# Kernel optimization log

Measured on AMD Instinct MI355X. Metric: run time of the kernel, lower is better.

## Reference

```python
import jax, jax.numpy as jnp
import numpy as np

NUM_HEADS = 16
GROUP_SIZE = 4
RMS_EPS = 1e-6


def _rope_cos_sin(S, head_dim):
    # matches compute_freqs_cis: freqs = 1/10000**(arange(0,hd,2)/hd), angles = outer(t, freqs)
    inv_freq = 1.0 / (10000.0 ** (jnp.arange(0, head_dim, 2, dtype=jnp.float32) / head_dim))
    t = jnp.arange(S, dtype=jnp.float32)
    angles = t[:, None] * inv_freq[None, :]          # [S, hd/2]
    return jnp.cos(angles), jnp.sin(angles)


def _apply_rope(x, cos, sin):
    # x: [B, S, h, hd]; complex multiply on (even, odd) pairs
    B, S, h, hd = x.shape
    xr = x.reshape(B, S, h, hd // 2, 2)
    x0, x1 = xr[..., 0], xr[..., 1]
    c = cos[None, :, None, :]
    s = sin[None, :, None, :]
    o0 = x0 * c - x1 * s
    o1 = x0 * s + x1 * c
    return jnp.stack([o0, o1], axis=-1).reshape(B, S, h, hd)


def setup_inputs() -> dict:
    key = jax.random.key(0)
    k1, k2, k3 = jax.random.split(key, 3)
    B, S, H = 4, 2048, 2048
    g = GROUP_SIZE
    x = jax.random.normal(k1, (B, S, H), dtype=jnp.float32)
    w_attn = jax.random.normal(k2, (H, H + 2 * H // g), dtype=jnp.float32) * 0.02
    w_proj = jax.random.normal(k3, (H, H), dtype=jnp.float32) * 0.02
    norm_w = jnp.ones((H,), dtype=jnp.float32)
    return {"x": x, "w_attn": w_attn, "w_proj": w_proj, "norm_w": norm_w}


def reference(x, w_attn, w_proj, norm_w):
    B, S, H = x.shape
    nh = NUM_HEADS
    g = GROUP_SIZE
    nkv = nh // g
    hd = H // nh
    ghd = H // g

    qkv = jnp.einsum('bsh,hf->bsf', x, w_attn)
    q = qkv[..., :H].reshape(B, S, nh, hd)
    k = qkv[..., H:H + ghd].reshape(B, S, nkv, hd)
    v = qkv[..., H + ghd:].reshape(B, S, nkv, hd)

    cos, sin = _rope_cos_sin(S, hd)
    q = _apply_rope(q, cos, sin)
    k = _apply_rope(k, cos, sin)

    q = q.transpose(0, 2, 1, 3)                      # [B, nh, S, hd]
    k = jnp.repeat(k.transpose(0, 2, 1, 3), g, axis=1)   # [B, nh, S, hd]
    v = jnp.repeat(v.transpose(0, 2, 1, 3), g, axis=1)

    scale = 1.0 / jnp.sqrt(jnp.float32(hd))
    scores = jnp.einsum('bhqd,bhkd->bhqk', q, k) * scale
    causal = jnp.tril(jnp.ones((S, S), dtype=bool))
    scores = jnp.where(causal[None, None], scores, jnp.finfo(scores.dtype).min)
    attn = jax.nn.softmax(scores, axis=-1)
    y = jnp.einsum('bhqk,bhkd->bhqd', attn, v)       # [B, nh, S, hd]
    y = y.transpose(0, 2, 1, 3).reshape(B, S, H)

    y = jnp.einsum('bsh,ho->bso', y, w_proj)
    # RMSNorm
    rms = jnp.sqrt(jnp.mean(jnp.square(y), axis=-1, keepdims=True) + RMS_EPS)
    return (y / rms) * norm_w
```

## Files before the change

kernel.cpp:

```cpp
#include <hip/hip_runtime.h>

#define DEVI __device__ __forceinline__

using u16 = unsigned short;
using u32 = unsigned int;

typedef __attribute__((ext_vector_type(8))) short short8v;
typedef __attribute__((ext_vector_type(4))) float f32x4;
typedef __attribute__((ext_vector_type(16))) float f32x16;
typedef __attribute__((ext_vector_type(2))) u32 u32x2;
typedef __attribute__((ext_vector_type(4))) u32 u32x4;

DEVI u16 f2b(float f) {
  u32 u = __builtin_bit_cast(u32, f);
  u += 0x7fffu + ((u >> 16) & 1u);
  return (u16)(u >> 16);
}
DEVI float b2f(u16 b) { return __builtin_bit_cast(float, (u32)b << 16); }

DEVI void gload16(const void* g, void* l) {
  __builtin_amdgcn_global_load_lds(
      (const __attribute__((address_space(1))) void*)g,
      (__attribute__((address_space(3))) void*)l, 16, 0, 0);
}

__global__ __launch_bounds__(256) void cvt_x_k(const float* __restrict__ in,
                                               u16* __restrict__ out) {
  size_t i = ((size_t)blockIdx.x * 256 + threadIdx.x) * 8;
  f32x4 a = *(const f32x4*)(in + i);
  f32x4 c = *(const f32x4*)(in + i + 4);
  short8v o;
  o[0] = (short)f2b(a[0]); o[1] = (short)f2b(a[1]);
  o[2] = (short)f2b(a[2]); o[3] = (short)f2b(a[3]);
  o[4] = (short)f2b(c[0]); o[5] = (short)f2b(c[1]);
  o[6] = (short)f2b(c[2]); o[7] = (short)f2b(c[3]);
  *(short8v*)(out + i) = o;
}

__global__ __launch_bounds__(256) void transpose_cvt_k(
    const float* __restrict__ in, u16* __restrict__ out, int R, int Ccols) {
  __shared__ u16 tile[64][65];
  const int r0 = blockIdx.y * 64, c0 = blockIdx.x * 64;
  const int tx = threadIdx.x & 63, ty = threadIdx.x >> 6;
#pragma unroll
  for (int jj = 0; jj < 16; ++jj) {
    int r = ty + jj * 4;
    tile[r][tx] = f2b(in[(size_t)(r0 + r) * Ccols + c0 + tx]);
  }
  __syncthreads();
#pragma unroll
  for (int jj = 0; jj < 16; ++jj) {
    int c = ty + jj * 4;
    out[(size_t)(c0 + c) * R + r0 + tx] = tile[tx][c];
  }
}

__global__ __launch_bounds__(256) void rope_table_k(float* __restrict__ cosT,
                                                    float* __restrict__ sinT) {
  int idx = blockIdx.x * 256 + threadIdx.x;
  int s = idx >> 6, i = idx & 63;
  float inv_freq = expf(-(float)i * (1.0f / 64.0f) * 9.210340371976184f);
  float ang = (float)s * inv_freq;
  cosT[idx] = cosf(ang);
  sinT[idx] = sinf(ang);
}

__global__ __launch_bounds__(256) void rope_scatter_k(
    const u16* __restrict__ qkv, const float* __restrict__ cosT,
    const float* __restrict__ sinT, u16* __restrict__ q_r,
    u16* __restrict__ k_r) {
  const float QS = 0.08838834764831845f * 1.4426950408889634f;
  const int row = blockIdx.x;
  const int b = row >> 11, s = row & 2047;
  const u16* in = qkv + (size_t)row * 3072;
  const float* cp = cosT + s * 64;
  const float* sp = sinT + s * 64;
  for (int p = threadIdx.x; p < 1280; p += 256) {
    int f0 = p * 2;
    u32 pair = *(const u32*)(in + f0);
    float x0 = b2f((u16)(pair & 0xffffu));
    float x1 = b2f((u16)(pair >> 16));
    int d, head;
    u16* dst;
    bool isq = (f0 < 2048);
    if (isq) {
      head = f0 >> 7; d = f0 & 127;
      dst = q_r + (((size_t)(b * 16 + head)) * 2048 + s) * 128 + d;
    } else {
      int idx = f0 - 2048;
      head = idx >> 7; d = idx & 127;
      dst = k_r + (((size_t)(b * 4 + head)) * 2048 + s) * 128 + d;
    }
    int i = d >> 1;
    float c = cp[i], sn = sp[i];
    float o0 = x0 * c - x1 * sn;
    float o1 = x0 * sn + x1 * c;
    if (isq) { o0 *= QS; o1 *= QS; }
    *(u32*)dst = (u32)f2b(o0) | ((u32)f2b(o1) << 16);
  }
}

__global__ __launch_bounds__(256) void v_trans_k(const u16* __restrict__ qkv,
                                                 u16* __restrict__ vT) {
  __shared__ u16 tile[64][65];
  const int s0 = blockIdx.x * 64, d0 = blockIdx.y * 64;
  const int bk = blockIdx.z;
  const int b = bk >> 2, kh = bk & 3;
  const int tx = threadIdx.x & 63, ty = threadIdx.x >> 6;
  const u16* src = qkv + ((size_t)b * 2048) * 3072 + 2560 + kh * 128;
#pragma unroll
  for (int jj = 0; jj < 16; ++jj) {
    int s = ty + jj * 4;
    tile[s][tx] = src[(size_t)(s0 + s) * 3072 + d0 + tx];
  }
  __syncthreads();
  u16* dst = vT + (((size_t)bk * 128 + d0) * 2048) + s0;
#pragma unroll
  for (int jj = 0; jj < 16; ++jj) {
    int dd = ty + jj * 4;
    dst[(size_t)dd * 2048 + tx] = tile[tx][dd];
  }
}

DEVI short8v ldf(const char* half, int r, int slot) {
  return *(const short8v*)(half + r * 64 + (((slot) ^ (r & 3)) << 4));
}

DEVI void stg(const u16* __restrict__ G, int row0, int Kd, int T, int kh,
              char* dst, int t, int w) {
#pragma unroll
  for (int i = 0; i < 2; ++i) {
    int off = i * 8192 + t * 16;
    int r = off >> 6;
    int gs = ((off >> 4) & 3) ^ (r & 3);
    gload16((const char*)G +
                (((size_t)(row0 + r) * Kd) + T * 64 + kh * 32 + gs * 8) * 2,
            dst + i * 8192 + w * 1024);
  }
}

#define VM4 asm volatile("s_waitcnt vmcnt(4)" ::: "memory")
#define PH(P2, KS, CH, STAGE_STMT, TAILWAIT)                                   \
  {                                                                            \
    if ((CH) == 0) {                                                           \
      _Pragma("unroll") for (int mt = 0; mt < 8; ++mt) af[mt] =                \
          ldf(Ab + (P2) * 32768 + (KS) * 16384, wm * 128 + mt * 16 + lo, hi);  \
    }                                                                          \
    bf0 = ldf(Bb + (P2) * 32768 + (KS) * 16384, wn * 64 + (CH) * 32 + lo, hi);\
    bf1 = ldf(Bb + (P2) * 32768 + (KS) * 16384,                                \
              wn * 64 + (CH) * 32 + 16 + lo, hi);                              \
    STAGE_STMT;                                                                \
    __builtin_amdgcn_sched_barrier(0);                                         \
    __builtin_amdgcn_s_barrier();                                              \
    asm volatile("s_waitcnt lgkmcnt(0)" ::: "memory");                         \
    __builtin_amdgcn_sched_barrier(0);                                         \
    __builtin_amdgcn_s_setprio(1);                                             \
    _Pragma("unroll") for (int mt = 0; mt < 8; ++mt) {                         \
      acc[mt][(CH) * 2] = __builtin_amdgcn_mfma_f32_16x16x32_bf16(             \
          af[mt], bf0, acc[mt][(CH) * 2], 0, 0, 0);                            \
      acc[mt][(CH) * 2 + 1] = __builtin_amdgcn_mfma_f32_16x16x32_bf16(         \
          af[mt], bf1, acc[mt][(CH) * 2 + 1], 0, 0, 0);                        \
    }                                                                          \
    __builtin_amdgcn_s_setprio(0);                                             \
    TAILWAIT;                                                                  \
    __builtin_amdgcn_sched_barrier(0);                                         \
    __builtin_amdgcn_s_barrier();                                              \
    __builtin_amdgcn_sched_barrier(0);                                         \
  }

__global__ __launch_bounds__(512, 2) void gemm256_k(const u16* __restrict__ A,
                                                    const u16* __restrict__ BT,
                                                    u16* __restrict__ C, int N,
                                                    int Kd) {
  __shared__ __align__(16) char lds[131072];
  char* Ab = lds;
  char* Bb = lds + 65536;

  const int t = threadIdx.x;
  const int lane = t & 63, lo = lane & 15, hi = lane >> 4;
  const int w = t >> 6, wm = w >> 2, wn = w & 3;

  const int ntx = gridDim.x;
  const int nwg = ntx * gridDim.y;
  const int orig = blockIdx.y * ntx + blockIdx.x;
  const int cpx = nwg >> 3;
  const int swz = (orig & 7) * cpx + (orig >> 3);
  const int m0 = (swz / ntx) * 256, n0 = (swz % ntx) * 256;

  f32x4 acc[8][4];
#pragma unroll
  for (int a = 0; a < 8; ++a)
#pragma unroll
    for (int c = 0; c < 4; ++c) acc[a][c] = (f32x4){0.f, 0.f, 0.f, 0.f};

  short8v af[8], bf0, bf1;

  const int NK = Kd >> 6;
  const int NK2 = NK >> 1;

  stg(A, m0, Kd, 0, 0, Ab + 0, t, w);
  stg(BT, n0, Kd, 0, 0, Bb + 0, t, w);
  stg(A, m0, Kd, 0, 1, Ab + 16384, t, w);
  stg(BT, n0, Kd, 0, 1, Bb + 16384, t, w);
  stg(A, m0, Kd, 1, 0, Ab + 32768, t, w);
  stg(BT, n0, Kd, 1, 0, Bb + 32768, t, w);
  VM4;
  __builtin_amdgcn_sched_barrier(0);
  __builtin_amdgcn_s_barrier();
  __builtin_amdgcn_sched_barrier(0);

  for (int kt2 = 0; kt2 < NK2; ++kt2) {
    int T1v = 2 * kt2 + 1;
    int T2v = 2 * kt2 + 2; if (T2v > NK - 1) T2v = NK - 1;
    int T3v = 2 * kt2 + 3; if (T3v > NK - 1) T3v = NK - 1;
    PH(0, 0, 0, stg(A, m0, Kd, T1v, 1, Ab + 49152, t, w), (void)0);
    PH(0, 0, 1, stg(BT, n0, Kd, T1v, 1, Bb + 49152, t, w), (void)0);
    PH(0, 1, 0, stg(A, m0, Kd, T2v, 0, Ab + 0, t, w), (void)0);
    PH(0, 1, 1, stg(BT, n0, Kd, T2v, 0, Bb + 0, t, w), VM4);
    PH(1, 0, 0, stg(A, m0, Kd, T2v, 1, Ab + 16384, t, w), (void)0);
    PH(1, 0, 1, stg(BT, n0, Kd, T2v, 1, Bb + 16384, t, w), (void)0);
    PH(1, 1, 0, stg(A, m0, Kd, T3v, 0, Ab + 32768, t, w), (void)0);
    PH(1, 1, 1, stg(BT, n0, Kd, T3v, 0, Bb + 32768, t, w), VM4);
  }
  asm volatile("s_waitcnt vmcnt(0)" ::: "memory");

#pragma unroll
  for (int mt = 0; mt < 8; ++mt)
#pragma unroll
    for (int nt = 0; nt < 4; ++nt)
#pragma unroll
      for (int r = 0; r < 4; ++r) {
        int row = m0 + wm * 128 + mt * 16 + hi * 4 + r;
        int col = n0 + wn * 64 + nt * 16 + lo;
        C[(size_t)row * N + col] = f2b(acc[mt][nt][r]);
      }
}

__global__ __launch_bounds__(256, 2) void attn_k(const u16* __restrict__ Q,
                                                 const u16* __restrict__ K,
                                                 const u16* __restrict__ VT,
                                                 u16* __restrict__ Y) {
  __shared__ __align__(16) u16 lK[2][64 * 128];
  __shared__ __align__(16) u16 lV[2][128 * 64];

  const int t = threadIdx.x;
  const int lane = t & 63;
  const int l31 = lane & 31, hb = lane >> 5;
  const int w = t >> 6;

  const int id = blockIdx.x;
  const int xcd = id & 7, pos = id >> 3;
  const int bh = xcd + ((pos >> 4) << 3);
  const int qt = 15 - (pos & 15);
  const int b = bh >> 4, h = bh & 15, kh = h >> 2;

  const size_t qbase = (size_t)(b * 16 + h) * 2048 * 128;
  const size_t kbase = (size_t)(b * 4 + kh) * 2048 * 128;
  const size_t vbase = (size_t)(b * 4 + kh) * 128 * 2048;

  const int q0 = qt * 128;
  const int qrow = q0 + w * 32 + l31;

  short8v qf[8];
#pragma unroll
  for (int j16 = 0; j16 < 8; ++j16)
    qf[j16] = *(const short8v*)(Q + qbase + (size_t)qrow * 128 + j16 * 16 + hb * 8);

  float m_run = -3.0e38f, l_run = 0.f;
  f32x16 oacc[4];
#pragma unroll
  for (int db = 0; db < 4; ++db)
#pragma unroll
    for (int rg = 0; rg < 16; ++rg) oacc[db][rg] = 0.f;

  const int ntile = 2 * qt + 2;

  auto stageK = [&](int buf, int j) {
    const int kv0 = j * 64;
#pragma unroll
    for (int i = 0; i < 4; ++i) {
      int off = i * 4096 + t * 16;
      int r = off >> 8;
      int sl = (off >> 4) & 15;
      int gs = sl ^ (r & 7);
      gload16((const char*)K + (kbase + (size_t)(kv0 + r) * 128 + gs * 8) * 2,
              (char*)lK[buf] + i * 4096 + w * 1024);
    }
  };
  auto stageV = [&](int buf, int j) {
    const int kv0 = j * 64;
#pragma unroll
    for (int i = 0; i < 4; ++i) {
      int off = i * 4096 + t * 16;
      int r = off >> 7;
      int sl = (off >> 4) & 7;
      int gs = sl ^ (r & 7);
      gload16((const char*)VT + (vbase + (size_t)r * 2048 + kv0 + gs * 8) * 2,
              (char*)lV[buf] + i * 4096 + w * 1024);
    }
  };

  auto pv = [&](const char* lVc, const short8v* pa) {
    __builtin_amdgcn_s_setprio(1);
#pragma unroll
    for (int sc = 0; sc < 4; ++sc) {
      const int c = sc * 2 + hb;
#pragma unroll
      for (int db = 0; db < 4; ++db) {
        int vr = db * 32 + l31;
        short8v vf = *(const short8v*)(lVc + vr * 128 + ((c ^ (vr & 7)) << 4));
        oacc[db] = __builtin_amdgcn_mfma_f32_32x32x16_bf16(vf, pa[sc],
                                                           oacc[db], 0, 0, 0);
      }
    }
    __builtin_amdgcn_s_setprio(0);
  };

  stageK(0, 0);
  asm volatile("s_waitcnt vmcnt(0)" ::: "memory");
  __builtin_amdgcn_sched_barrier(0);
  __builtin_amdgcn_s_barrier();
  __builtin_amdgcn_sched_barrier(0);

  short8v pa_prev[4];

  for (int jj = 0; jj < ntile; ++jj) {
    const int cur = jj & 1;
    if (jj + 1 < ntile) stageK(cur ^ 1, jj + 1);
    stageV(cur, jj);

    const char* lKc = (const char*)lK[cur];
    const int kv0 = jj * 64;

    f32x16 sacc[2];
#pragma unroll
    for (int kb = 0; kb < 2; ++kb)
#pragma unroll
      for (int rg = 0; rg < 16; ++rg) sacc[kb][rg] = 0.f;

    __builtin_amdgcn_s_setprio(1);
#pragma unroll
    for (int j16 = 0; j16 < 8; ++j16) {
      const int c = j16 * 2 + hb;
#pragma unroll
      for (int kb = 0; kb < 2; ++kb) {
        int kr = kb * 32 + l31;
        short8v kf = *(const short8v*)(lKc + kr * 256 + ((c ^ (kr & 7)) << 4));
        sacc[kb] = __builtin_amdgcn_mfma_f32_32x32x16_bf16(kf, qf[j16],
                                                           sacc[kb], 0, 0, 0);
      }
    }
    __builtin_amdgcn_s_setprio(0);

    if (jj >= ntile - 2) {
      const int mb = kv0 + 4 * hb - qrow;
#pragma unroll
      for (int kb = 0; kb < 2; ++kb)
#pragma unroll
        for (int rg = 0; rg < 16; ++rg)
          if (mb + kb * 32 + (rg & 3) + 8 * (rg >> 2) > 0)
            sacc[kb][rg] = -1.0e38f;
    }

    float mt0[16];
#pragma unroll
    for (int rg = 0; rg < 16; ++rg) mt0[rg] = fmaxf(sacc[0][rg], sacc[1][rg]);
#pragma unroll
    for (int rg = 0; rg < 8; ++rg) mt0[rg] = fmaxf(mt0[rg], mt0[rg + 8]);
#pragma unroll
    for (int rg = 0; rg < 4; ++rg) mt0[rg] = fmaxf(mt0[rg], mt0[rg + 4]);
    float mx = fmaxf(fmaxf(mt0[0], mt0[1]), fmaxf(mt0[2], mt0[3]));
    mx = fmaxf(mx, __shfl_xor(mx, 32, 64));

    if (jj > 0) pv((const char*)lV[cur ^ 1], pa_prev);

    if (__any(mx > m_run + 8.f)) {
      float mn = fmaxf(m_run, mx);
      float corr = exp2f(m_run - mn);
      m_run = mn;
      l_run *= corr;
#pragma unroll
      for (int db = 0; db < 4; ++db)
#pragma unroll
        for (int rg = 0; rg < 16; ++rg) oacc[db][rg] *= corr;
    }

    float sm0[16];
#pragma unroll
    for (int kb = 0; kb < 2; ++kb)
#pragma unroll
      for (int rg = 0; rg < 16; ++rg)
        sacc[kb][rg] = exp2f(sacc[kb][rg] - m_run);
#pragma unroll
    for (int rg = 0; rg < 16; ++rg) sm0[rg] = sacc[0][rg] + sacc[1][rg];
#pragma unroll
    for (int rg = 0; rg < 8; ++rg) sm0[rg] += sm0[rg + 8];
#pragma unroll
    for (int rg = 0; rg < 4; ++rg) sm0[rg] += sm0[rg + 4];
    float sm = (sm0[0] + sm0[1]) + (sm0[2] + sm0[3]);
    sm += __shfl_xor(sm, 32, 64);
    l_run += sm;

#pragma unroll
    for (int kb = 0; kb < 2; ++kb) {
      u32 pw00, pw01, pw10, pw11, pw20, pw21, pw30, pw31;
      asm("v_cvt_pk_bf16_f32 %0, %1, %2" : "=v"(pw00) : "v"(sacc[kb][0]), "v"(sacc[kb][1]));
      asm("v_cvt_pk_bf16_f32 %0, %1, %2" : "=v"(pw01) : "v"(sacc[kb][2]), "v"(sacc[kb][3]));
      asm("v_cvt_pk_bf16_f32 %0, %1, %2" : "=v"(pw10) : "v"(sacc[kb][4]), "v"(sacc[kb][5]));
      asm("v_cvt_pk_bf16_f32 %0, %1, %2" : "=v"(pw11) : "v"(sacc[kb][6]), "v"(sacc[kb][7]));
      asm("v_cvt_pk_bf16_f32 %0, %1, %2" : "=v"(pw20) : "v"(sacc[kb][8]), "v"(sacc[kb][9]));
      asm("v_cvt_pk_bf16_f32 %0, %1, %2" : "=v"(pw21) : "v"(sacc[kb][10]), "v"(sacc[kb][11]));
      asm("v_cvt_pk_bf16_f32 %0, %1, %2" : "=v"(pw30) : "v"(sacc[kb][12]), "v"(sacc[kb][13]));
      asm("v_cvt_pk_bf16_f32 %0, %1, %2" : "=v"(pw31) : "v"(sacc[kb][14]), "v"(sacc[kb][15]));
      u32x2 a0 = __builtin_amdgcn_permlane32_swap(pw00, pw10, false, false);
      u32x2 a1 = __builtin_amdgcn_permlane32_swap(pw01, pw11, false, false);
      u32x4 wv0; wv0[0] = a0[0]; wv0[1] = a1[0]; wv0[2] = a0[1]; wv0[3] = a1[1];
      pa_prev[kb * 2 + 0] = __builtin_bit_cast(short8v, wv0);
      u32x2 b0 = __builtin_amdgcn_permlane32_swap(pw20, pw30, false, false);
      u32x2 b1 = __builtin_amdgcn_permlane32_swap(pw21, pw31, false, false);
      u32x4 wv1; wv1[0] = b0[0]; wv1[1] = b1[0]; wv1[2] = b0[1]; wv1[3] = b1[1];
      pa_prev[kb * 2 + 1] = __builtin_bit_cast(short8v, wv1);
    }

    asm volatile("s_waitcnt vmcnt(0)" ::: "memory");
    __builtin_amdgcn_sched_barrier(0);
    __builtin_amdgcn_s_barrier();
    __builtin_amdgcn_sched_barrier(0);
  }

  pv((const char*)lV[(ntile - 1) & 1], pa_prev);

  const float inv = 1.0f / l_run;
  u16* yp = Y + ((size_t)b * 2048 + qrow) * 2048 + h * 128;
#pragma unroll
  for (int db = 0; db < 4; ++db)
#pragma unroll
    for (int j = 0; j < 4; ++j) {
      float a0 = oacc[db][4 * j] * inv, a1 = oacc[db][4 * j + 1] * inv;
      float a2 = oacc[db][4 * j + 2] * inv, a3 = oacc[db][4 * j + 3] * inv;
      u32 w0, w1;
      asm("v_cvt_pk_bf16_f32 %0, %1, %2" : "=v"(w0) : "v"(a0), "v"(a1));
      asm("v_cvt_pk_bf16_f32 %0, %1, %2" : "=v"(w1) : "v"(a2), "v"(a3));
      *(u32x2*)(yp + db * 32 + 8 * j + 4 * hb) = (u32x2){w0, w1};
    }
}

__global__ __launch_bounds__(256) void rmsnorm_k(const u16* __restrict__ Yb,
                                                 const float* __restrict__ nw,
                                                 float* __restrict__ out) {
  const int row = blockIdx.x;
  const int t = threadIdx.x;
  const u16* yr = Yb + (size_t)row * 2048 + t * 8;
  short8v v = *(const short8v*)yr;
  float x[8];
  float ss = 0.f;
#pragma unroll
  for (int j = 0; j < 8; ++j) {
    x[j] = b2f((u16)v[j]);
    ss += x[j] * x[j];
  }
#pragma unroll
  for (int dm = 1; dm < 64; dm <<= 1) ss += __shfl_xor(ss, dm, 64);
  __shared__ float red[4];
  if ((t & 63) == 0) red[t >> 6] = ss;
  __syncthreads();
  float tot = red[0] + red[1] + red[2] + red[3];
  float inv = rsqrtf(tot * (1.0f / 2048.0f) + 1e-6f);
  float* op = out + (size_t)row * 2048 + t * 8;
  const float* wp = nw + t * 8;
  f32x4 o0, o1;
#pragma unroll
  for (int j = 0; j < 4; ++j) o0[j] = x[j] * inv * wp[j];
#pragma unroll
  for (int j = 0; j < 4; ++j) o1[j] = x[4 + j] * inv * wp[4 + j];
  *(f32x4*)op = o0;
  *(f32x4*)(op + 4) = o1;
}

extern "C" void kernel_launch(void* const* d_in, const int* in_sizes, int n_in,
                              void* d_out, int out_size, void* d_ws,
                              size_t ws_size, hipStream_t stream) {
  (void)in_sizes; (void)n_in; (void)out_size; (void)ws_size;
  const float* x = (const float*)d_in[0];
  const float* w_attn = (const float*)d_in[1];
  const float* w_proj = (const float*)d_in[2];
  const float* norm_w = (const float*)d_in[3];
  float* out = (float*)d_out;
  char* ws = (char*)d_ws;

  size_t off = 0;
  auto alloc = [&](size_t n) {
    size_t r = off;
    off += (n + 255) & ~(size_t)255;
    return r;
  };
  u16* xb = (u16*)(ws + alloc(33554432));
  u16* wabT = (u16*)(ws + alloc(12582912));
  u16* qkv = (u16*)(ws + alloc(50331648));
  u16* q_r = (u16*)(ws + alloc(33554432));
  u16* vT = (u16*)(ws + alloc(8388608));
  u16* wpT = (u16*)(ws + alloc(8388608));
  float* cosT = (float*)(ws + alloc(524288));
  float* sinT = (float*)(ws + alloc(524288));
  u16* k_r = wabT;
  u16* y = xb;
  u16* y2 = qkv;

  cvt_x_k<<<8192, 256, 0, stream>>>(x, xb);
  transpose_cvt_k<<<dim3(48, 32), 256, 0, stream>>>(w_attn, wabT, 2048, 3072);
  transpose_cvt_k<<<dim3(32, 32), 256, 0, stream>>>(w_proj, wpT, 2048, 2048);
  rope_table_k<<<512, 256, 0, stream>>>(cosT, sinT);
  gemm256_k<<<dim3(12, 32), 512, 0, stream>>>(xb, wabT, qkv, 3072, 2048);
  rope_scatter_k<<<8192, 256, 0, stream>>>(qkv, cosT, sinT, q_r, k_r);
  v_trans_k<<<dim3(32, 2, 16), 256, 0, stream>>>(qkv, vT);
  attn_k<<<dim3(1024), 256, 0, stream>>>(q_r, k_r, vT, y);
  gemm256_k<<<dim3(8, 32), 512, 0, stream>>>(y, wpT, y2, 2048, 2048);
  rmsnorm_k<<<8192, 256, 0, stream>>>(y2, norm_w, out);
}
```

Before: 408.2 us.

## Use 512-thread attention blocks with 256-row Q tiles and triple-buffered K/V prefetch

The attention kernel now runs 8 waves per block, each block covering 256 query rows, so every K/V tile staged into LDS is shared by twice as many waves. K and V are prefetched two tiles ahead into a three-slot ring buffer with partial vmcnt waits, replacing the old double buffer that drained all loads each iteration. The deferred PV of the previous tile is replaced by an in-iteration PV on the current tile. This cuts global K/V traffic and barrier stalls, but gives one block per CU, larger LDS use, coarser causal load balance (512 blocks), and less overlap between softmax and MFMA.

```diff
diff --git a/kernel.cpp b/kernel.cpp
--- a/kernel.cpp
+++ b/kernel.cpp
@@ -236,12 +236,12 @@
       }
 }
 
-__global__ __launch_bounds__(256, 2) void attn_k(const u16* __restrict__ Q,
+__global__ __launch_bounds__(512, 1) void attn_k(const u16* __restrict__ Q,
                                                  const u16* __restrict__ K,
                                                  const u16* __restrict__ VT,
                                                  u16* __restrict__ Y) {
-  __shared__ __align__(16) u16 lK[2][64 * 128];
-  __shared__ __align__(16) u16 lV[2][128 * 64];
+  __shared__ __align__(16) u16 lK[3][64 * 128];
+  __shared__ __align__(16) u16 lV[3][128 * 64];
 
   const int t = threadIdx.x;
   const int lane = t & 63;
@@ -250,15 +250,15 @@
 
   const int id = blockIdx.x;
   const int xcd = id & 7, pos = id >> 3;
-  const int bh = xcd + ((pos >> 4) << 3);
-  const int qt = 15 - (pos & 15);
+  const int bh = xcd + ((pos >> 3) << 3);
+  const int qt = 7 - (pos & 7);
   const int b = bh >> 4, h = bh & 15, kh = h >> 2;
 
   const size_t qbase = (size_t)(b * 16 + h) * 2048 * 128;
   const size_t kbase = (size_t)(b * 4 + kh) * 2048 * 128;
   const size_t vbase = (size_t)(b * 4 + kh) * 128 * 2048;
 
-  const int q0 = qt * 128;
+  const int q0 = qt * 256;
   const int qrow = q0 + w * 32 + l31;
 
   short8v qf[8];
@@ -273,63 +273,53 @@
 #pragma unroll
     for (int rg = 0; rg < 16; ++rg) oacc[db][rg] = 0.f;
 
-  const int ntile = 2 * qt + 2;
+  const int ntile = 4 * qt + 4;
 
   auto stageK = [&](int buf, int j) {
     const int kv0 = j * 64;
 #pragma unroll
-    for (int i = 0; i < 4; ++i) {
-      int off = i * 4096 + t * 16;
+    for (int i = 0; i < 2; ++i) {
+      int off = i * 8192 + t * 16;
       int r = off >> 8;
       int sl = (off >> 4) & 15;
       int gs = sl ^ (r & 7);
       gload16((const char*)K + (kbase + (size_t)(kv0 + r) * 128 + gs * 8) * 2,
-              (char*)lK[buf] + i * 4096 + w * 1024);
+              (char*)lK[buf] + i * 8192 + w * 1024);
     }
   };
   auto stageV = [&](int buf, int j) {
     const int kv0 = j * 64;
 #pragma unroll
-    for (int i = 0; i < 4; ++i) {
-      int off = i * 4096 + t * 16;
+    for (int i = 0; i < 2; ++i) {
+      int off = i * 8192 + t * 16;
       int r = off >> 7;
       int sl = (off >> 4) & 7;
       int gs = sl ^ (r & 7);
       gload16((const char*)VT + (vbase + (size_t)r * 2048 + kv0 + gs * 8) * 2,
-              (char*)lV[buf] + i * 4096 + w * 1024);
+              (char*)lV[buf] + i * 8192 + w * 1024);
     }
   };
 
-  auto pv = [&](const char* lVc, const short8v* pa) {
-    __builtin_amdgcn_s_setprio(1);
-#pragma unroll
-    for (int sc = 0; sc < 4; ++sc) {
-      const int c = sc * 2 + hb;
-#pragma unroll
-      for (int db = 0; db < 4; ++db) {
-        int vr = db * 32 + l31;
-        short8v vf = *(const short8v*)(lVc + vr * 128 + ((c ^ (vr & 7)) << 4));
-        oacc[db] = __builtin_amdgcn_mfma_f32_32x32x16_bf16(vf, pa[sc],
-                                                           oacc[db], 0, 0, 0);
-      }
-    }
-    __builtin_amdgcn_s_setprio(0);
-  };
-
   stageK(0, 0);
-  asm volatile("s_waitcnt vmcnt(0)" ::: "memory");
+  stageV(0, 0);
+  if (ntile > 1) { stageK(1, 1); stageV(1, 1); }
+  if (ntile > 1) { asm volatile("s_waitcnt vmcnt(4)" ::: "memory"); }
+  else           { asm volatile("s_waitcnt vmcnt(0)" ::: "memory"); }
   __builtin_amdgcn_sched_barrier(0);
   __builtin_amdgcn_s_barrier();
   __builtin_amdgcn_sched_barrier(0);
 
-  short8v pa_prev[4];
-
+  int buf = 0;
   for (int jj = 0; jj < ntile; ++jj) {
-    const int cur = jj & 1;
-    if (jj + 1 < ntile) stageK(cur ^ 1, jj + 1);
-    stageV(cur, jj);
-
-    const char* lKc = (const char*)lK[cur];
+    const bool iss = (jj + 2 < ntile);
+    if (iss) {
+      int nb = buf + 2; if (nb >= 3) nb -= 3;
+      stageK(nb, jj + 2);
+      stageV(nb, jj + 2);
+    }
+
+    const char* lKc = (const char*)lK[buf];
+    const char* lVc = (const char*)lV[buf];
     const int kv0 = jj * 64;
 
     f32x16 sacc[2];
@@ -352,7 +342,7 @@
     }
     __builtin_amdgcn_s_setprio(0);
 
-    if (jj >= ntile - 2) {
+    if (jj >= ntile - 4) {
       const int mb = kv0 + 4 * hb - qrow;
 #pragma unroll
       for (int kb = 0; kb < 2; ++kb)
@@ -371,8 +361,6 @@
     for (int rg = 0; rg < 4; ++rg) mt0[rg] = fmaxf(mt0[rg], mt0[rg + 4]);
     float mx = fmaxf(fmaxf(mt0[0], mt0[1]), fmaxf(mt0[2], mt0[3]));
     mx = fmaxf(mx, __shfl_xor(mx, 32, 64));
-
-    if (jj > 0) pv((const char*)lV[cur ^ 1], pa_prev);
 
     if (__any(mx > m_run + 8.f)) {
       float mn = fmaxf(m_run, mx);
@@ -401,6 +389,7 @@
     sm += __shfl_xor(sm, 32, 64);
     l_run += sm;
 
+    short8v pa[4];
 #pragma unroll
     for (int kb = 0; kb < 2; ++kb) {
       u32 pw00, pw01, pw10, pw11, pw20, pw21, pw30, pw31;
@@ -415,20 +404,35 @@
       u32x2 a0 = __builtin_amdgcn_permlane32_swap(pw00, pw10, false, false);
       u32x2 a1 = __builtin_amdgcn_permlane32_swap(pw01, pw11, false, false);
       u32x4 wv0; wv0[0] = a0[0]; wv0[1] = a1[0]; wv0[2] = a0[1]; wv0[3] = a1[1];
-      pa_prev[kb * 2 + 0] = __builtin_bit_cast(short8v, wv0);
+      pa[kb * 2 + 0] = __builtin_bit_cast(short8v, wv0);
       u32x2 b0 = __builtin_amdgcn_permlane32_swap(pw20, pw30, false, false);
       u32x2 b1 = __builtin_amdgcn_permlane32_swap(pw21, pw31, false, false);
       u32x4 wv1; wv1[0] = b0[0]; wv1[1] = b1[0]; wv1[2] = b0[1]; wv1[3] = b1[1];
-      pa_prev[kb * 2 + 1] = __builtin_bit_cast(short8v, wv1);
-    }
-
-    asm volatile("s_waitcnt vmcnt(0)" ::: "memory");
+      pa[kb * 2 + 1] = __builtin_bit_cast(short8v, wv1);
+    }
+
+    __builtin_amdgcn_s_setprio(1);
+#pragma unroll
+    for (int sc = 0; sc < 4; ++sc) {
+      const int c = sc * 2 + hb;
+#pragma unroll
+      for (int db = 0; db < 4; ++db) {
+        int vr = db * 32 + l31;
+        short8v vf = *(const short8v*)(lVc + vr * 128 + ((c ^ (vr & 7)) << 4));
+        oacc[db] = __builtin_amdgcn_mfma_f32_32x32x16_bf16(vf, pa[sc],
+                                                           oacc[db], 0, 0, 0);
+      }
+    }
+    __builtin_amdgcn_s_setprio(0);
+
+    if (iss) { asm volatile("s_waitcnt vmcnt(4)" ::: "memory"); }
+    else     { asm volatile("s_waitcnt vmcnt(0)" ::: "memory"); }
     __builtin_amdgcn_sched_barrier(0);
     __builtin_amdgcn_s_barrier();
     __builtin_amdgcn_sched_barrier(0);
-  }
-
-  pv((const char*)lV[(ntile - 1) & 1], pa_prev);
+
+    ++buf; if (buf >= 3) buf = 0;
+  }
 
   const float inv = 1.0f / l_run;
   u16* yp = Y + ((size_t)b * 2048 + qrow) * 2048 + h * 128;
@@ -513,7 +517,7 @@
   gemm256_k<<<dim3(12, 32), 512, 0, stream>>>(xb, wabT, qkv, 3072, 2048);
   rope_scatter_k<<<8192, 256, 0, stream>>>(qkv, cosT, sinT, q_r, k_r);
   v_trans_k<<<dim3(32, 2, 16), 256, 0, stream>>>(qkv, vT);
-  attn_k<<<dim3(1024), 256, 0, stream>>>(q_r, k_r, vT, y);
+  attn_k<<<dim3(512), 512, 0, stream>>>(q_r, k_r, vT, y);
   gemm256_k<<<dim3(8, 32), 512, 0, stream>>>(y, wpT, y2, 2048, 2048);
   rmsnorm_k<<<8192, 256, 0, stream>>>(y2, norm_w, out);
 }
```

New measurement: 445.3 us. +9.1%, slower.

## Drop LDS staging in attention kernel, load K/V directly from global

Applied to the files above, without the earlier changes.

Removes the shared-memory double buffering of K and V tiles and the per-tile barriers. Each wave now reads K and V fragments straight from global memory, relying on the L2 cache. The block-to-head mapping is also changed so that the four query heads sharing a KV head sit on the same XCD, which improves L2 reuse. In exchange, K/V reuse across waves now depends on the cache, global load latency is exposed to the MFMA loop, and the PV product is no longer software-pipelined one tile behind.

```diff
diff --git a/kernel.cpp b/kernel.cpp
--- a/kernel.cpp
+++ b/kernel.cpp
@@ -240,23 +240,21 @@
                                                  const u16* __restrict__ K,
                                                  const u16* __restrict__ VT,
                                                  u16* __restrict__ Y) {
-  __shared__ __align__(16) u16 lK[2][64 * 128];
-  __shared__ __align__(16) u16 lV[2][128 * 64];
-
   const int t = threadIdx.x;
   const int lane = t & 63;
   const int l31 = lane & 31, hb = lane >> 5;
   const int w = t >> 6;
 
   const int id = blockIdx.x;
-  const int xcd = id & 7, pos = id >> 3;
-  const int bh = xcd + ((pos >> 4) << 3);
-  const int qt = 15 - (pos & 15);
-  const int b = bh >> 4, h = bh & 15, kh = h >> 2;
+  const int xcd = id & 7, idx = id >> 3;
+  const int pair = xcd * 2 + (idx >> 6);
+  const int b = pair >> 2, kh = pair & 3;
+  const int h = kh * 4 + ((idx >> 4) & 3);
+  const int qt = 15 - (idx & 15);
 
   const size_t qbase = (size_t)(b * 16 + h) * 2048 * 128;
-  const size_t kbase = (size_t)(b * 4 + kh) * 2048 * 128;
-  const size_t vbase = (size_t)(b * 4 + kh) * 128 * 2048;
+  const u16* Kp = K + (size_t)(b * 4 + kh) * 2048 * 128;
+  const u16* Vp = VT + (size_t)(b * 4 + kh) * 128 * 2048;
 
   const int q0 = qt * 128;
   const int qrow = q0 + w * 32 + l31;
@@ -275,77 +273,22 @@
 
   const int ntile = 2 * qt + 2;
 
-  auto stageK = [&](int buf, int j) {
-    const int kv0 = j * 64;
-#pragma unroll
-    for (int i = 0; i < 4; ++i) {
-      int off = i * 4096 + t * 16;
-      int r = off >> 8;
-      int sl = (off >> 4) & 15;
-      int gs = sl ^ (r & 7);
-      gload16((const char*)K + (kbase + (size_t)(kv0 + r) * 128 + gs * 8) * 2,
-              (char*)lK[buf] + i * 4096 + w * 1024);
-    }
-  };
-  auto stageV = [&](int buf, int j) {
-    const int kv0 = j * 64;
-#pragma unroll
-    for (int i = 0; i < 4; ++i) {
-      int off = i * 4096 + t * 16;
-      int r = off >> 7;
-      int sl = (off >> 4) & 7;
-      int gs = sl ^ (r & 7);
-      gload16((const char*)VT + (vbase + (size_t)r * 2048 + kv0 + gs * 8) * 2,
-              (char*)lV[buf] + i * 4096 + w * 1024);
-    }
-  };
-
-  auto pv = [&](const char* lVc, const short8v* pa) {
+  for (int jj = 0; jj < ntile; ++jj) {
+    const int kv0 = jj * 64;
+
+    f32x16 sacc[2];
+#pragma unroll
+    for (int kb = 0; kb < 2; ++kb)
+#pragma unroll
+      for (int rg = 0; rg < 16; ++rg) sacc[kb][rg] = 0.f;
+
     __builtin_amdgcn_s_setprio(1);
 #pragma unroll
-    for (int sc = 0; sc < 4; ++sc) {
-      const int c = sc * 2 + hb;
-#pragma unroll
-      for (int db = 0; db < 4; ++db) {
-        int vr = db * 32 + l31;
-        short8v vf = *(const short8v*)(lVc + vr * 128 + ((c ^ (vr & 7)) << 4));
-        oacc[db] = __builtin_amdgcn_mfma_f32_32x32x16_bf16(vf, pa[sc],
-                                                           oacc[db], 0, 0, 0);
-      }
-    }
-    __builtin_amdgcn_s_setprio(0);
-  };
-
-  stageK(0, 0);
-  asm volatile("s_waitcnt vmcnt(0)" ::: "memory");
-  __builtin_amdgcn_sched_barrier(0);
-  __builtin_amdgcn_s_barrier();
-  __builtin_amdgcn_sched_barrier(0);
-
-  short8v pa_prev[4];
-
-  for (int jj = 0; jj < ntile; ++jj) {
-    const int cur = jj & 1;
-    if (jj + 1 < ntile) stageK(cur ^ 1, jj + 1);
-    stageV(cur, jj);
-
-    const char* lKc = (const char*)lK[cur];
-    const int kv0 = jj * 64;
-
-    f32x16 sacc[2];
-#pragma unroll
-    for (int kb = 0; kb < 2; ++kb)
-#pragma unroll
-      for (int rg = 0; rg < 16; ++rg) sacc[kb][rg] = 0.f;
-
-    __builtin_amdgcn_s_setprio(1);
-#pragma unroll
     for (int j16 = 0; j16 < 8; ++j16) {
-      const int c = j16 * 2 + hb;
 #pragma unroll
       for (int kb = 0; kb < 2; ++kb) {
-        int kr = kb * 32 + l31;
-        short8v kf = *(const short8v*)(lKc + kr * 256 + ((c ^ (kr & 7)) << 4));
+        short8v kf = *(const short8v*)(Kp +
+            (size_t)(kv0 + kb * 32 + l31) * 128 + j16 * 16 + hb * 8);
         sacc[kb] = __builtin_amdgcn_mfma_f32_32x32x16_bf16(kf, qf[j16],
                                                            sacc[kb], 0, 0, 0);
       }
@@ -371,8 +314,6 @@
     for (int rg = 0; rg < 4; ++rg) mt0[rg] = fmaxf(mt0[rg], mt0[rg + 4]);
     float mx = fmaxf(fmaxf(mt0[0], mt0[1]), fmaxf(mt0[2], mt0[3]));
     mx = fmaxf(mx, __shfl_xor(mx, 32, 64));
-
-    if (jj > 0) pv((const char*)lV[cur ^ 1], pa_prev);
 
     if (__any(mx > m_run + 8.f)) {
       float mn = fmaxf(m_run, mx);
@@ -401,6 +342,7 @@
     sm += __shfl_xor(sm, 32, 64);
     l_run += sm;
 
+    short8v pa[4];
 #pragma unroll
     for (int kb = 0; kb < 2; ++kb) {
       u32 pw00, pw01, pw10, pw11, pw20, pw21, pw30, pw31;
@@ -415,20 +357,26 @@
       u32x2 a0 = __builtin_amdgcn_permlane32_swap(pw00, pw10, false, false);
       u32x2 a1 = __builtin_amdgcn_permlane32_swap(pw01, pw11, false, false);
       u32x4 wv0; wv0[0] = a0[0]; wv0[1] = a1[0]; wv0[2] = a0[1]; wv0[3] = a1[1];
-      pa_prev[kb * 2 + 0] = __builtin_bit_cast(short8v, wv0);
+      pa[kb * 2 + 0] = __builtin_bit_cast(short8v, wv0);
       u32x2 b0 = __builtin_amdgcn_permlane32_swap(pw20, pw30, false, false);
       u32x2 b1 = __builtin_amdgcn_permlane32_swap(pw21, pw31, false, false);
       u32x4 wv1; wv1[0] = b0[0]; wv1[1] = b1[0]; wv1[2] = b0[1]; wv1[3] = b1[1];
-      pa_prev[kb * 2 + 1] = __builtin_bit_cast(short8v, wv1);
-    }
-
-    asm volatile("s_waitcnt vmcnt(0)" ::: "memory");
-    __builtin_amdgcn_sched_barrier(0);
-    __builtin_amdgcn_s_barrier();
-    __builtin_amdgcn_sched_barrier(0);
-  }
-
-  pv((const char*)lV[(ntile - 1) & 1], pa_prev);
+      pa[kb * 2 + 1] = __builtin_bit_cast(short8v, wv1);
+    }
+
+    __builtin_amdgcn_s_setprio(1);
+#pragma unroll
+    for (int sc = 0; sc < 4; ++sc) {
+#pragma unroll
+      for (int db = 0; db < 4; ++db) {
+        short8v vf = *(const short8v*)(Vp +
+            (size_t)(db * 32 + l31) * 2048 + kv0 + sc * 16 + hb * 8);
+        oacc[db] = __builtin_amdgcn_mfma_f32_32x32x16_bf16(vf, pa[sc],
+                                                           oacc[db], 0, 0, 0);
+      }
+    }
+    __builtin_amdgcn_s_setprio(0);
+  }
 
   const float inv = 1.0f / l_run;
   u16* yp = Y + ((size_t)b * 2048 + qrow) * 2048 + h * 128;
```

After: 636.2 us. 55.9% more time.

## Use 128-wide KV tiles in attention and drop the software-pipelined PV step

Applied to the files above, without the earlier changes.

The attention kernel now processes 128 keys per iteration instead of 64, staging both K and V tiles together into double-buffered LDS. This halves loop iterations, barriers and softmax reductions per key. It removes the deferred PV matmul that overlapped the previous tile's PV with the current QK. LDS usage grows to 128KB and launch bounds drop to one block per CU, so occupancy and latency hiding may suffer, and register pressure rises with 4 score accumulators and 8 P fragments.

```diff
diff --git a/kernel.cpp b/kernel.cpp
--- a/kernel.cpp
+++ b/kernel.cpp
@@ -236,12 +236,12 @@
       }
 }
 
-__global__ __launch_bounds__(256, 2) void attn_k(const u16* __restrict__ Q,
+__global__ __launch_bounds__(256, 1) void attn_k(const u16* __restrict__ Q,
                                                  const u16* __restrict__ K,
                                                  const u16* __restrict__ VT,
                                                  u16* __restrict__ Y) {
-  __shared__ __align__(16) u16 lK[2][64 * 128];
-  __shared__ __align__(16) u16 lV[2][128 * 64];
+  __shared__ __align__(16) u16 lK[2][128 * 128];
+  __shared__ __align__(16) u16 lV[2][128 * 128];
 
   const int t = threadIdx.x;
   const int lane = t & 63;
@@ -273,12 +273,12 @@
 #pragma unroll
     for (int rg = 0; rg < 16; ++rg) oacc[db][rg] = 0.f;
 
-  const int ntile = 2 * qt + 2;
-
-  auto stageK = [&](int buf, int j) {
-    const int kv0 = j * 64;
-#pragma unroll
-    for (int i = 0; i < 4; ++i) {
+  const int ntile = qt + 1;
+
+  auto stage = [&](int buf, int j) {
+    const int kv0 = j * 128;
+#pragma unroll
+    for (int i = 0; i < 8; ++i) {
       int off = i * 4096 + t * 16;
       int r = off >> 8;
       int sl = (off >> 4) & 15;
@@ -286,55 +286,34 @@
       gload16((const char*)K + (kbase + (size_t)(kv0 + r) * 128 + gs * 8) * 2,
               (char*)lK[buf] + i * 4096 + w * 1024);
     }
-  };
-  auto stageV = [&](int buf, int j) {
-    const int kv0 = j * 64;
-#pragma unroll
-    for (int i = 0; i < 4; ++i) {
+#pragma unroll
+    for (int i = 0; i < 8; ++i) {
       int off = i * 4096 + t * 16;
-      int r = off >> 7;
-      int sl = (off >> 4) & 7;
+      int r = off >> 8;
+      int sl = (off >> 4) & 15;
       int gs = sl ^ (r & 7);
       gload16((const char*)VT + (vbase + (size_t)r * 2048 + kv0 + gs * 8) * 2,
               (char*)lV[buf] + i * 4096 + w * 1024);
     }
   };
 
-  auto pv = [&](const char* lVc, const short8v* pa) {
-    __builtin_amdgcn_s_setprio(1);
-#pragma unroll
-    for (int sc = 0; sc < 4; ++sc) {
-      const int c = sc * 2 + hb;
-#pragma unroll
-      for (int db = 0; db < 4; ++db) {
-        int vr = db * 32 + l31;
-        short8v vf = *(const short8v*)(lVc + vr * 128 + ((c ^ (vr & 7)) << 4));
-        oacc[db] = __builtin_amdgcn_mfma_f32_32x32x16_bf16(vf, pa[sc],
-                                                           oacc[db], 0, 0, 0);
-      }
-    }
-    __builtin_amdgcn_s_setprio(0);
-  };
-
-  stageK(0, 0);
+  stage(0, 0);
   asm volatile("s_waitcnt vmcnt(0)" ::: "memory");
   __builtin_amdgcn_sched_barrier(0);
   __builtin_amdgcn_s_barrier();
   __builtin_amdgcn_sched_barrier(0);
 
-  short8v pa_prev[4];
-
   for (int jj = 0; jj < ntile; ++jj) {
     const int cur = jj & 1;
-    if (jj + 1 < ntile) stageK(cur ^ 1, jj + 1);
-    stageV(cur, jj);
+    if (jj + 1 < ntile) stage(cur ^ 1, jj + 1);
 
     const char* lKc = (const char*)lK[cur];
-    const int kv0 = jj * 64;
-
-    f32x16 sacc[2];
-#pragma unroll
-    for (int kb = 0; kb < 2; ++kb)
+    const char* lVc = (const char*)lV[cur];
+    const int kv0 = jj * 128;
+
+    f32x16 sacc[4];
+#pragma unroll
+    for (int kb = 0; kb < 4; ++kb)
 #pragma unroll
       for (int rg = 0; rg < 16; ++rg) sacc[kb][rg] = 0.f;
 
@@ -343,7 +322,7 @@
     for (int j16 = 0; j16 < 8; ++j16) {
       const int c = j16 * 2 + hb;
 #pragma unroll
-      for (int kb = 0; kb < 2; ++kb) {
+      for (int kb = 0; kb < 4; ++kb) {
         int kr = kb * 32 + l31;
         short8v kf = *(const short8v*)(lKc + kr * 256 + ((c ^ (kr & 7)) << 4));
         sacc[kb] = __builtin_amdgcn_mfma_f32_32x32x16_bf16(kf, qf[j16],
@@ -352,10 +331,10 @@
     }
     __builtin_amdgcn_s_setprio(0);
 
-    if (jj >= ntile - 2) {
+    if (jj == ntile - 1) {
       const int mb = kv0 + 4 * hb - qrow;
 #pragma unroll
-      for (int kb = 0; kb < 2; ++kb)
+      for (int kb = 0; kb < 4; ++kb)
 #pragma unroll
         for (int rg = 0; rg < 16; ++rg)
           if (mb + kb * 32 + (rg & 3) + 8 * (rg >> 2) > 0)
@@ -364,15 +343,15 @@
 
     float mt0[16];
 #pragma unroll
-    for (int rg = 0; rg < 16; ++rg) mt0[rg] = fmaxf(sacc[0][rg], sacc[1][rg]);
+    for (int rg = 0; rg < 16; ++rg)
+      mt0[rg] = fmaxf(fmaxf(sacc[0][rg], sacc[1][rg]),
+                      fmaxf(sacc[2][rg], sacc[3][rg]));
 #pragma unroll
     for (int rg = 0; rg < 8; ++rg) mt0[rg] = fmaxf(mt0[rg], mt0[rg + 8]);
 #pragma unroll
     for (int rg = 0; rg < 4; ++rg) mt0[rg] = fmaxf(mt0[rg], mt0[rg + 4]);
     float mx = fmaxf(fmaxf(mt0[0], mt0[1]), fmaxf(mt0[2], mt0[3]));
     mx = fmaxf(mx, __shfl_xor(mx, 32, 64));
-
-    if (jj > 0) pv((const char*)lV[cur ^ 1], pa_prev);
 
     if (__any(mx > m_run + 8.f)) {
       float mn = fmaxf(m_run, mx);
@@ -387,12 +366,13 @@
 
     float sm0[16];
 #pragma unroll
-    for (int kb = 0; kb < 2; ++kb)
+    for (int kb = 0; kb < 4; ++kb)
 #pragma unroll
       for (int rg = 0; rg < 16; ++rg)
         sacc[kb][rg] = exp2f(sacc[kb][rg] - m_run);
 #pragma unroll
-    for (int rg = 0; rg < 16; ++rg) sm0[rg] = sacc[0][rg] + sacc[1][rg];
+    for (int rg = 0; rg < 16; ++rg)
+      sm0[rg] = (sacc[0][rg] + sacc[1][rg]) + (sacc[2][rg] + sacc[3][rg]);
 #pragma unroll
     for (int rg = 0; rg < 8; ++rg) sm0[rg] += sm0[rg + 8];
 #pragma unroll
@@ -401,8 +381,9 @@
     sm += __shfl_xor(sm, 32, 64);
     l_run += sm;
 
-#pragma unroll
-    for (int kb = 0; kb < 2; ++kb) {
+    short8v pa[8];
+#pragma unroll
+    for (int kb = 0; kb < 4; ++kb) {
       u32 pw00, pw01, pw10, pw11, pw20, pw21, pw30, pw31;
       asm("v_cvt_pk_bf16_f32 %0, %1, %2" : "=v"(pw00) : "v"(sacc[kb][0]), "v"(sacc[kb][1]));
       asm("v_cvt_pk_bf16_f32 %0, %1, %2" : "=v"(pw01) : "v"(sacc[kb][2]), "v"(sacc[kb][3]));
@@ -415,20 +396,32 @@
       u32x2 a0 = __builtin_amdgcn_permlane32_swap(pw00, pw10, false, false);
       u32x2 a1 = __builtin_amdgcn_permlane32_swap(pw01, pw11, false, false);
       u32x4 wv0; wv0[0] = a0[0]; wv0[1] = a1[0]; wv0[2] = a0[1]; wv0[3] = a1[1];
-      pa_prev[kb * 2 + 0] = __builtin_bit_cast(short8v, wv0);
+      pa[kb * 2 + 0] = __builtin_bit_cast(short8v, wv0);
       u32x2 b0 = __builtin_amdgcn_permlane32_swap(pw20, pw30, false, false);
       u32x2 b1 = __builtin_amdgcn_permlane32_swap(pw21, pw31, false, false);
       u32x4 wv1; wv1[0] = b0[0]; wv1[1] = b1[0]; wv1[2] = b0[1]; wv1[3] = b1[1];
-      pa_prev[kb * 2 + 1] = __builtin_bit_cast(short8v, wv1);
-    }
+      pa[kb * 2 + 1] = __builtin_bit_cast(short8v, wv1);
+    }
+
+    __builtin_amdgcn_s_setprio(1);
+#pragma unroll
+    for (int sc = 0; sc < 8; ++sc) {
+      const int c = sc * 2 + hb;
+#pragma unroll
+      for (int db = 0; db < 4; ++db) {
+        int vr = db * 32 + l31;
+        short8v vf = *(const short8v*)(lVc + vr * 256 + (((c & 15) ^ (vr & 7)) << 4));
+        oacc[db] = __builtin_amdgcn_mfma_f32_32x32x16_bf16(vf, pa[sc],
+                                                           oacc[db], 0, 0, 0);
+      }
+    }
+    __builtin_amdgcn_s_setprio(0);
 
     asm volatile("s_waitcnt vmcnt(0)" ::: "memory");
     __builtin_amdgcn_sched_barrier(0);
     __builtin_amdgcn_s_barrier();
     __builtin_amdgcn_sched_barrier(0);
   }
-
-  pv((const char*)lV[(ntile - 1) & 1], pa_prev);
 
   const float inv = 1.0f / l_run;
   u16* yp = Y + ((size_t)b * 2048 + qrow) * 2048 + h * 128;
```

Result: slower. 478.4 us (+17.2%).
